# Kernel tuning notes

Hardware: AMD Instinct MI355X
Metric: run time of the kernel (lower is better)

Reference implementation:

```python
import jax, jax.numpy as jnp
import numpy as np

N = 10000       # nodes (atoms)
E = 160000      # edges (avg degree 16)
NE = 10         # num_elements
C = 64          # hidden scalar channels (hidden_irreps 0e multiplicity)
NB = 8          # num_bessel
SH = 9          # spherical-harmonic dim for max_ell=2 (1+3+5)
MLPH = 16       # readout MLP hidden (MLP_irreps)
T = 2           # num_interactions
R_MAX = 5.0
P_CUT = 6       # num_polynomial_cutoff
AVG_NEIGH = 32.0


def _sph(u):
    # real spherical harmonics up to l=2, e3nn 'component' normalization
    x, y, z = u[:, 0], u[:, 1], u[:, 2]
    s3, s5, s15 = 3.0 ** 0.5, 5.0 ** 0.5, 15.0 ** 0.5
    return jnp.stack([
        jnp.ones_like(x),
        s3 * x, s3 * y, s3 * z,
        s15 * x * y, s15 * y * z, (s5 / 2) * (3 * z * z - 1),
        s15 * x * z, (s15 / 2) * (x * x - y * y)], axis=-1)


def _radial(r):
    # Bessel radial basis * smooth polynomial cutoff (RadialEmbeddingBlock)
    n = jnp.arange(1, NB + 1, dtype=r.dtype)
    bessel = (2.0 / R_MAX) ** 0.5 * jnp.sin(n * jnp.pi * r[:, None] / R_MAX) / r[:, None]
    x = jnp.clip(r / R_MAX, 0.0, 1.0)
    p = P_CUT
    fc = (1.0 - 0.5 * (p + 1) * (p + 2) * x ** p
          + p * (p + 2) * x ** (p + 1)
          - 0.5 * p * (p + 1) * x ** (p + 2))
    fc = jnp.where(x < 1.0, fc, 0.0)
    return bessel * fc[:, None]


def setup_inputs():
    key = jax.random.key(0)
    ks = jax.random.split(key, 14)
    positions = jax.random.normal(ks[0], (N, 3), jnp.float32) * 3.0
    node_attrs = jax.nn.one_hot(jax.random.randint(ks[1], (N,), 0, NE), NE, dtype=jnp.float32)
    edge_index = jax.random.randint(ks[2], (2, E), 0, N)
    shifts = jnp.zeros((E, 3), jnp.float32)

    def g(k, shape, fan):
        return jax.random.normal(k, shape, jnp.float32) / np.sqrt(fan)

    params = dict(
        atomic_energies=jax.random.normal(ks[3], (NE,), jnp.float32),
        W_embed=g(ks[4], (NE, C), NE),          # LinearNodeEmbeddingBlock
        W_up=g(ks[5], (T, C, C), C),            # linear_up per interaction
        W_r1=g(ks[6], (T, NB, MLPH), NB),       # radial MLP layer 1
        W_r2=g(ks[7], (T, MLPH, C * SH), MLPH), # radial MLP -> TP weights
        W_mix=g(ks[8], (T, C, SH, C), C * SH),  # post-scatter linear mixing
        W_self=g(ks[9], (T, C, C), C),          # self/skip connection
        w_read=g(ks[10], (C,), C),              # LinearReadoutBlock
        W_mlp1=g(ks[11], (C, MLPH), C),         # NonLinearReadoutBlock
        w_mlp2=g(ks[12], (MLPH,), MLPH),
    )
    return dict(positions=positions, node_attrs=node_attrs, shifts=shifts,
                edge_index=edge_index, **params)


def reference(positions, node_attrs, shifts, atomic_energies, W_embed, W_up,
              W_r1, W_r2, W_mix, W_self, w_read, W_mlp1, w_mlp2, edge_index):
    snd, rcv = edge_index[0], edge_index[1]
    vec = positions[rcv] - positions[snd] + shifts              # [E,3]
    r = jnp.linalg.norm(vec, axis=-1) + 1e-9                    # [E]
    sh = _sph(vec / r[:, None])                                 # [E,SH]
    edge_feats = _radial(r)                                     # [E,NB]

    h = node_attrs @ W_embed                                    # [N,C] node embedding
    reps = [node_attrs @ atomic_energies]                       # node_e0
    for t in range(T):
        h_up = h @ W_up[t]                                      # [N,C]
        # radial-MLP produced tensor-product weights, one per (channel, sh) path
        tp_w = (jax.nn.silu(edge_feats @ W_r1[t]) @ W_r2[t]).reshape(-1, C, SH)
        # gather -> edge-wise tensor product -> scatter-reduce (the hot loop)
        msg = tp_w * h_up[snd][:, :, None] * sh[:, None, :]     # [E,C,SH]
        agg = jax.ops.segment_sum(msg, rcv, num_segments=N) / AVG_NEIGH
        h = jnp.einsum('ncs,cso->no', agg, W_mix[t]) + h @ W_self[t]
        if t < T - 1:
            reps.append(h @ w_read)                             # linear readout
        else:
            reps.append(jax.nn.silu(h @ W_mlp1) @ w_mlp2)       # nonlinear readout
    return jnp.stack(reps, axis=0)  # [T+1, N] per-layer atomic energy contributions
```

## Files before the change

kernel.cpp:

```cpp
#include <hip/hip_runtime.h>
#include <math.h>

#define N_NODES 10000
#define N_EDGES 160000
#define NEL 10
#define C 64
#define NB 8
#define SHD 9
#define MLPH 16
#define CSH 576
#define R_MAX 5.0f
#define INV_AVG 0.03125f
#define SCAN_CH 40
#define ROWP  584
#define NPB   8

typedef _Float16 f16x2 __attribute__((ext_vector_type(2)));
typedef _Float16 f16x8 __attribute__((ext_vector_type(8)));
typedef float    f32x4 __attribute__((ext_vector_type(4)));
typedef _Float16 half_t;

__device__ __forceinline__ float silu_f(float v) {
    return v / (1.0f + __expf(-v));
}

__device__ __forceinline__ float dot2f(f16x2 a, f16x2 b, float c) {
#if __has_builtin(__builtin_amdgcn_fdot2)
    return __builtin_amdgcn_fdot2(a, b, c, false);
#else
    return c + (float)a.x * (float)b.x + (float)a.y * (float)b.y;
#endif
}

__global__ __launch_bounds__(256) void k_zero(
    int* __restrict__ cnt, int* __restrict__ deg)
{
    int i = blockIdx.x * 256 + threadIdx.x;
    if (i == 0) *cnt = 0;
    if (i < N_NODES) deg[i] = 0;
}

__global__ __launch_bounds__(256) void k_edge(
    const float* __restrict__ pos, const float* __restrict__ shifts,
    const int* __restrict__ ei,
    const float* __restrict__ na, const float* __restrict__ We,
    const float* __restrict__ ae,
    const float* __restrict__ Wr2, const float* __restrict__ Wmix,
    const float* __restrict__ Wself, const float* __restrict__ Wup,
    int* __restrict__ cnt, int* __restrict__ deg,
    int* __restrict__ act_snd, int* __restrict__ act_rcv,
    float* __restrict__ act_u, float* __restrict__ act_ef,
    f16x2* __restrict__ wlth, f16x8* __restrict__ wmixf, f16x8* __restrict__ wupf,
    half_t* __restrict__ hh, float* __restrict__ out)
{
    int i = blockIdx.x * 256 + threadIdx.x;
    int lane = threadIdx.x & 63;

    {
        int n = i >> 6;
        float acc = 0.0f, e0 = 0.0f;
        #pragma unroll
        for (int k = 0; k < NEL; k++) {
            float a = na[n * NEL + k];
            acc += a * We[k * C + lane];
            e0 += a * ae[k];
        }
        hh[i] = (half_t)acc;
        if (lane == 0) out[n] = e0;
    }

    if (blockIdx.x >= N_EDGES / 256) {
        int idx = i - N_EDGES;
        if (idx < 2 * 8 * CSH) {
            int t = idx / (8 * CSH);
            int r = idx - t * (8 * CSH);
            int mq = r / CSH, j = r - mq * CSH;
            int c = j & 63, s = j >> 6;
            float lo = Wr2[t * MLPH * CSH + (2 * mq + 0) * CSH + c * SHD + s];
            float hi = Wr2[t * MLPH * CSH + (2 * mq + 1) * CSH + c * SHD + s];
            f16x2 v; v.x = (_Float16)lo; v.y = (_Float16)hi;
            wlth[idx] = v;
        } else if (idx < 2 * 8 * CSH + 10240) {
            int k2 = idx - 2 * 8 * CSH;
            int t = k2 / 5120;
            int r = k2 - t * 5120;
            int ks = r >> 8;
            int rr = r & 255;
            int nt = rr >> 6;
            int ln = rr & 63;
            f16x8 v;
            #pragma unroll
            for (int e = 0; e < 8; e++) {
                int k = ks * 32 + ((ln >> 4) << 3) + e;
                int col = nt * 16 + (ln & 15);
                float x;
                if (k < CSH)
                    x = Wmix[(size_t)t * CSH * C + ((k & 63) * SHD + (k >> 6)) * C + col] * INV_AVG;
                else
                    x = Wself[(size_t)t * C * C + (k - CSH) * C + col];
                v[e] = (_Float16)x;
            }
            wmixf[(size_t)((t * 20 + ks) * 4 + nt) * 64 + ln] = v;
        } else if (idx < 2 * 8 * CSH + 10240 + 1024) {
            int k2 = idx - (2 * 8 * CSH + 10240);
            int t = k2 >> 9;
            int r = k2 & 511;
            int ks = r >> 8;
            int rr = r & 255;
            int nt = rr >> 6;
            int ln = rr & 63;
            f16x8 v;
            #pragma unroll
            for (int e = 0; e < 8; e++) {
                int k = ks * 32 + ((ln >> 4) << 3) + e;
                int col = nt * 16 + (ln & 15);
                v[e] = (_Float16)Wup[(size_t)t * C * C + k * C + col];
            }
            wupf[(size_t)((t * 2 + ks) * 4 + nt) * 64 + ln] = v;
        }
        return;
    }

    int e = i;
    int snd = ei[e];
    int rcv = ei[N_EDGES + e];
    float vx = pos[rcv * 3 + 0] - pos[snd * 3 + 0] + shifts[e * 3 + 0];
    float vy = pos[rcv * 3 + 1] - pos[snd * 3 + 1] + shifts[e * 3 + 1];
    float vz = pos[rcv * 3 + 2] - pos[snd * 3 + 2] + shifts[e * 3 + 2];
    float r = sqrtf(vx * vx + vy * vy + vz * vz) + 1e-9f;
    float x = r / R_MAX;
    bool active = x < 1.0f;

    unsigned long long m = __ballot(active);
    int base = 0;
    if (m) {
        int leader = __ffsll((unsigned long long)m) - 1;
        if (lane == leader) base = atomicAdd(cnt, __popcll(m));
        base = __shfl(base, leader);
    }
    if (!active) return;

    int p = base + __popcll(m & ((1ull << lane) - 1ull));
    act_snd[p] = snd;
    act_rcv[p] = rcv;
    atomicAdd(&deg[rcv], 1);

    float inv_r = 1.0f / r;
    *(float4*)&act_u[p * 4] = make_float4(vx * inv_r, vy * inv_r, vz * inv_r, r);

    float x6 = x * x * x; x6 = x6 * x6;
    float x7 = x6 * x;
    float x8 = x7 * x;
    float fc = 1.0f - 28.0f * x6 + 48.0f * x7 - 21.0f * x8;
    float theta = 3.14159265358979323846f * r / R_MAX;
    float s1 = sinf(theta), c1 = cosf(theta);
    float sn = s1, cn = c1;
    float scale = 0.6324555320336759f * inv_r * fc;
    float ef[NB];
    ef[0] = scale * sn;
    #pragma unroll
    for (int n = 1; n < NB; n++) {
        float sn1 = sn * c1 + cn * s1;
        float cn1 = cn * c1 - sn * s1;
        sn = sn1; cn = cn1;
        ef[n] = scale * sn;
    }
    *(float4*)&act_ef[p * 8 + 0] = make_float4(ef[0], ef[1], ef[2], ef[3]);
    *(float4*)&act_ef[p * 8 + 4] = make_float4(ef[4], ef[5], ef[6], ef[7]);
}

__global__ __launch_bounds__(256) void k_scan(
    const int* __restrict__ deg, int* __restrict__ rowptr, int* __restrict__ cursor)
{
    __shared__ int dl[N_NODES];
    __shared__ int part[256];
    int tid = threadIdx.x;
    for (int i = tid; i < N_NODES; i += 256) dl[i] = deg[i];
    __syncthreads();

    int base = tid * SCAN_CH;
    int s = 0;
    #pragma unroll 8
    for (int i = 0; i < SCAN_CH; i++) {
        int idx = base + i;
        if (idx < N_NODES) s += dl[idx];
    }
    part[tid] = s;
    __syncthreads();
    for (int off = 1; off < 256; off <<= 1) {
        int v = (tid >= off) ? part[tid - off] : 0;
        __syncthreads();
        part[tid] += v;
        __syncthreads();
    }
    int run = part[tid] - s;
    for (int i = 0; i < SCAN_CH; i++) {
        int idx = base + i;
        if (idx < N_NODES) {
            int v = dl[idx];
            dl[idx] = run;
            run += v;
        }
    }
    __syncthreads();
    for (int i = tid; i < N_NODES; i += 256) {
        int r = dl[i];
        rowptr[i] = r;
        cursor[i] = r;
    }
    if (tid == 255) rowptr[N_NODES] = part[255];
}

__global__ __launch_bounds__(256) void k_scatter(
    const int* __restrict__ cnt, const int* __restrict__ act_snd,
    const int* __restrict__ act_rcv, const float* __restrict__ act_u,
    const float* __restrict__ act_ef, const float* __restrict__ Wr1,
    int* __restrict__ cursor,
    int* __restrict__ csnd, int* __restrict__ crcv, float* __restrict__ csh,
    f16x2* __restrict__ chidh0, f16x2* __restrict__ chidh1)
{
    int i = blockIdx.x * 256 + threadIdx.x;
    if (i >= *cnt) return;
    int rcv = act_rcv[i];
    int p = atomicAdd(&cursor[rcv], 1);

    csnd[p] = act_snd[i];
    crcv[p] = rcv;

    float4 u4 = *(const float4*)&act_u[i * 4];
    float ux = u4.x, uy = u4.y, uz = u4.z;
    const float s3 = 1.7320508075688772f;
    const float s5 = 2.23606797749979f;
    const float s15 = 3.872983346207417f;
    *(float4*)&csh[p * 16 + 0] = make_float4(1.0f, s3 * ux, s3 * uy, s3 * uz);
    *(float4*)&csh[p * 16 + 4] = make_float4(s15 * ux * uy, s15 * uy * uz,
                                             0.5f * s5 * (3.0f * uz * uz - 1.0f),
                                             s15 * ux * uz);
    csh[p * 16 + 8] = 0.5f * s15 * (ux * ux - uy * uy);

    float4 e0 = *(const float4*)&act_ef[i * 8 + 0];
    float4 e1 = *(const float4*)&act_ef[i * 8 + 4];
    float ef[NB] = {e0.x, e0.y, e0.z, e0.w, e1.x, e1.y, e1.z, e1.w};

    #pragma unroll
    for (int t = 0; t < 2; t++) {
        f16x2* dst = (t == 0) ? chidh0 : chidh1;
        const float* W = Wr1 + t * NB * MLPH;
        f16x2 hv2[8];
        #pragma unroll
        for (int mp = 0; mp < 8; mp++) {
            float a0 = 0.0f, a1 = 0.0f;
            #pragma unroll
            for (int b = 0; b < NB; b++) {
                float efb = ef[b];
                a0 += efb * W[b * MLPH + 2 * mp + 0];
                a1 += efb * W[b * MLPH + 2 * mp + 1];
            }
            f16x2 v; v.x = (_Float16)silu_f(a0); v.y = (_Float16)silu_f(a1);
            hv2[mp] = v;
        }
        *(float4*)&dst[p * 8 + 0] = *(float4*)&hv2[0];
        *(float4*)&dst[p * 8 + 4] = *(float4*)&hv2[4];
    }
}

__global__ __launch_bounds__(64) void k_upm(
    const half_t* __restrict__ hh, const f16x8* __restrict__ wupf,
    float* __restrict__ hup)
{
    int lane = threadIdx.x & 63;
    int base = blockIdx.x * 16;
    int rowA = base + (lane & 15);
    int kg = (lane >> 4) << 3;

    f32x4 u0 = {0.f,0.f,0.f,0.f}, u1 = {0.f,0.f,0.f,0.f};
    f32x4 u2 = {0.f,0.f,0.f,0.f}, u3 = {0.f,0.f,0.f,0.f};
    const half_t* hrow = hh + (size_t)rowA * C + kg;
    #pragma unroll
    for (int ks = 0; ks < 2; ks++) {
        f16x8 a = *(const f16x8*)(hrow + ks * 32);
        const f16x8* bp = wupf + (size_t)(ks * 4) * 64 + lane;
        u0 = __builtin_amdgcn_mfma_f32_16x16x32_f16(a, bp[0],   u0, 0, 0, 0);
        u1 = __builtin_amdgcn_mfma_f32_16x16x32_f16(a, bp[64],  u1, 0, 0, 0);
        u2 = __builtin_amdgcn_mfma_f32_16x16x32_f16(a, bp[128], u2, 0, 0, 0);
        u3 = __builtin_amdgcn_mfma_f32_16x16x32_f16(a, bp[192], u3, 0, 0, 0);
    }
    int colb = lane & 15;
    int rowb = base + ((lane >> 4) << 2);
    #pragma unroll
    for (int r = 0; r < 4; r++) {
        float* hp = hup + (size_t)(rowb + r) * C + colb;
        hp[0]  = u0[r];
        hp[16] = u1[r];
        hp[32] = u2[r];
        hp[48] = u3[r];
    }
}

template <int RMODE>
__global__ __launch_bounds__(256) void k_fuse(
    const int* __restrict__ rowptr, const int* __restrict__ csnd,
    const int* __restrict__ crcv, const float* __restrict__ csh,
    const f16x2* __restrict__ chh, const f16x2* __restrict__ wlth,
    const float* __restrict__ hup_in, const f16x8* __restrict__ wf,
    const f16x8* __restrict__ wupf1, half_t* __restrict__ hh,
    const float* __restrict__ wread, const float* __restrict__ Wm1,
    const float* __restrict__ wm2,
    float* __restrict__ hup_out, float* __restrict__ rep)
{
    __shared__ half_t Hs[NPB * ROWP];
    __shared__ half_t Hs2[NPB * 72];
    __shared__ float  Hn[NPB * 68];
    __shared__ float  W1l[C * MLPH];

    int lane = threadIdx.x & 63;
    int w = threadIdx.x >> 6;
    int bbase = blockIdx.x * NPB;
    int n0 = bbase + w * 2;
    int beg = rowptr[n0], end = rowptr[n0 + 2];

    f16x2 wreg[8][9];
    #pragma unroll
    for (int mq = 0; mq < 8; mq++)
        #pragma unroll
        for (int jj = 0; jj < 9; jj++)
            wreg[mq][jj] = wlth[mq * CSH + (jj << 6) + lane];

    float acc[9];
    int curRcv = -1;

#define FLUSH() { half_t* ag = &Hs[(curRcv - bbase) * ROWP + lane]; \
    _Pragma("unroll") for (int jj = 0; jj < 9; jj++) ag[jj << 6] = (half_t)acc[jj]; }
#define ZFILL(FROM, TO) for (int zn = (FROM); zn < (TO); zn++) { \
    half_t* ag = &Hs[(zn - bbase) * ROWP + lane]; \
    _Pragma("unroll") for (int jj = 0; jj < 9; jj++) ag[jj << 6] = (half_t)0.0f; }

    for (int k0 = beg; k0 < end; k0 += 4) {
        int nv = end - k0; if (nv > 4) nv = 4;

#define PRE(Q) int kc##Q = (k0 + Q < end) ? k0 + Q : end - 1; \
        int rcvq##Q = crcv[kc##Q]; \
        float hupq##Q = hup_in[csnd[kc##Q] * C + lane];
        PRE(0) PRE(1) PRE(2) PRE(3)
#undef PRE

        float tw0[9], tw1[9], tw2[9], tw3[9];
        #pragma unroll
        for (int jj = 0; jj < 9; jj++) {
            tw0[jj] = 0.f; tw1[jj] = 0.f; tw2[jj] = 0.f; tw3[jj] = 0.f;
        }

        #pragma unroll
        for (int mq = 0; mq < 8; mq++) {
            f16x2 h0 = chh[kc0 * 8 + mq], h1 = chh[kc1 * 8 + mq];
            f16x2 h2 = chh[kc2 * 8 + mq], h3 = chh[kc3 * 8 + mq];
            #pragma unroll
            for (int jj = 0; jj < 9; jj++) {
                f16x2 wv = wreg[mq][jj];
                tw0[jj] = dot2f(h0, wv, tw0[jj]);
                tw1[jj] = dot2f(h1, wv, tw1[jj]);
                tw2[jj] = dot2f(h2, wv, tw2[jj]);
                tw3[jj] = dot2f(h3, wv, tw3[jj]);
            }
        }

#define SCAT(Q) if (Q < nv) { \
        int rcv = rcvq##Q; \
        float hupS = hupq##Q; \
        float4 sA = *(const float4*)&csh[kc##Q * 16]; \
        float4 sB = *(const float4*)&csh[kc##Q * 16 + 4]; \
        float s8v = csh[kc##Q * 16 + 8]; \
        float sh9[9] = {sA.x, sA.y, sA.z, sA.w, sB.x, sB.y, sB.z, sB.w, s8v}; \
        if (rcv != curRcv) { \
            if (curRcv >= 0) { FLUSH(); ZFILL(curRcv + 1, rcv) } else { ZFILL(n0, rcv) } \
            curRcv = rcv; \
            _Pragma("unroll") for (int jj = 0; jj < 9; jj++) acc[jj] = tw##Q[jj] * (hupS * sh9[jj]); \
        } else { \
            _Pragma("unroll") for (int jj = 0; jj < 9; jj++) acc[jj] += tw##Q[jj] * (hupS * sh9[jj]); \
        } }
        SCAT(0) SCAT(1) SCAT(2) SCAT(3)
#undef SCAT
    }

    int zfrom = n0;
    if (curRcv >= 0) { FLUSH(); zfrom = curRcv + 1; }
    ZFILL(zfrom, n0 + 2)
#undef FLUSH
#undef ZFILL

    __syncthreads();

    int rowL = lane & 15;
    int rowS = rowL & 7;
    int kg = (lane >> 4) << 3;
    f32x4 acc4 = {0.f, 0.f, 0.f, 0.f};
    const half_t* hrow = hh + (size_t)(bbase + rowS) * C + kg;
    #pragma unroll
    for (int ks = 0; ks < 20; ks++) {
        f16x8 a = (ks < 18) ? *(const f16x8*)&Hs[rowS * ROWP + ks * 32 + kg]
                            : *(const f16x8*)(hrow + (ks - 18) * 32);
        f16x8 b = wf[(size_t)(ks * 4 + w) * 64 + lane];
        acc4 = __builtin_amdgcn_mfma_f32_16x16x32_f16(a, b, acc4, 0, 0, 0);
    }

    int colb = lane & 15;
    int rq = (lane >> 4) << 2;
    bool storeR = rq < NPB;

    __syncthreads();

    if (RMODE == 0) {
        if (storeR) {
            #pragma unroll
            for (int r = 0; r < 4; r++)
                Hs2[(rq + r) * 72 + w * 16 + colb] = (half_t)acc4[r];
        }
        __syncthreads();

        if (w == 0) {
            int row = lane & 15, seg = lane >> 4;
            float v = 0.0f;
            if (row < NPB) {
                #pragma unroll
                for (int j = 0; j < 16; j++)
                    v += (float)Hs2[row * 72 + seg * 16 + j] * wread[seg * 16 + j];
            }
            v += __shfl_xor(v, 16);
            v += __shfl_xor(v, 32);
            if (seg == 0 && row < NPB) rep[bbase + row] = v;
        }

        {
            int idx = threadIdx.x;
            if (idx < 64) {
                int row = idx >> 3, cq = idx & 7;
                *(float4*)&hh[(size_t)(bbase + row) * C + cq * 8] =
                    *(const float4*)&Hs2[row * 72 + cq * 8];
            }
        }

        f32x4 u = {0.f, 0.f, 0.f, 0.f};
        #pragma unroll
        for (int ks = 0; ks < 2; ks++) {
            f16x8 a = *(const f16x8*)&Hs2[rowS * 72 + ks * 32 + kg];
            f16x8 b = wupf1[(size_t)(ks * 4 + w) * 64 + lane];
            u = __builtin_amdgcn_mfma_f32_16x16x32_f16(a, b, u, 0, 0, 0);
        }
        if (storeR) {
            #pragma unroll
            for (int r = 0; r < 4; r++)
                hup_out[(size_t)(bbase + rq + r) * C + w * 16 + colb] = u[r];
        }
    } else {
        for (int t = threadIdx.x; t < C * MLPH; t += 256) W1l[t] = Wm1[t];
        if (storeR) {
            #pragma unroll
            for (int r = 0; r < 4; r++)
                Hn[(rq + r) * 68 + w * 16 + colb] = acc4[r];
        }
        __syncthreads();

        int n = threadIdx.x >> 4, m = threadIdx.x & 15;
        if (n < NPB) {
            float a2 = 0.0f;
            #pragma unroll 8
            for (int c = 0; c < C; c++) a2 += Hn[n * 68 + c] * W1l[c * MLPH + m];
            float rv = silu_f(a2) * wm2[m];
            rv += __shfl_xor(rv, 1); rv += __shfl_xor(rv, 2);
            rv += __shfl_xor(rv, 4); rv += __shfl_xor(rv, 8);
            if (m == 0) rep[bbase + n] = rv;
        }
    }
}

extern "C" void kernel_launch(void* const* d_in, const int* in_sizes, int n_in,
                              void* d_out, int out_size, void* d_ws, size_t ws_size,
                              hipStream_t stream) {
    const float* pos    = (const float*)d_in[0];
    const float* na     = (const float*)d_in[1];
    const float* shifts = (const float*)d_in[2];
    const int*   ei     = (const int*)d_in[3];
    const float* ae     = (const float*)d_in[4];
    const float* We     = (const float*)d_in[5];
    const float* Wup    = (const float*)d_in[6];
    const float* Wr1    = (const float*)d_in[7];
    const float* Wr2    = (const float*)d_in[8];
    const float* Wmix   = (const float*)d_in[9];
    const float* Wself  = (const float*)d_in[10];
    const float* wread  = (const float*)d_in[11];
    const float* Wm1    = (const float*)d_in[12];
    const float* wm2    = (const float*)d_in[13];
    float* out = (float*)d_out;

    char* ws = (char*)d_ws;
    size_t off = 0;
    auto alloc = [&](size_t bytes) {
        off = (off + 255) & ~(size_t)255;
        void* p = ws + off;
        off += bytes;
        return p;
    };
    int*   cnt     = (int*)alloc(4);
    int*   deg     = (int*)alloc((size_t)N_NODES * 4);
    int*   rowptr  = (int*)alloc((size_t)(N_NODES + 1) * 4);
    int*   cursor  = (int*)alloc((size_t)N_NODES * 4);
    f16x2* wlth    = (f16x2*)alloc((size_t)2 * 8 * CSH * 4);
    f16x8* wmixf   = (f16x8*)alloc((size_t)2 * 5120 * 16);
    f16x8* wupf    = (f16x8*)alloc((size_t)1024 * 16);
    int*   act_snd = (int*)alloc((size_t)N_EDGES * 4);
    int*   act_rcv = (int*)alloc((size_t)N_EDGES * 4);
    float* act_u   = (float*)alloc((size_t)N_EDGES * 4 * 4);
    float* act_ef  = (float*)alloc((size_t)N_EDGES * 8 * 4);
    int*   csnd    = (int*)alloc((size_t)N_EDGES * 4);
    int*   crcv    = (int*)alloc((size_t)N_EDGES * 4);
    float* csh     = (float*)alloc((size_t)N_EDGES * 16 * 4);
    f16x2* chidh0  = (f16x2*)alloc((size_t)N_EDGES * 8 * 4);
    f16x2* chidh1  = (f16x2*)alloc((size_t)N_EDGES * 8 * 4);
    float* hup     = (float*)alloc((size_t)N_NODES * C * 4);
    float* hup2    = (float*)alloc((size_t)N_NODES * C * 4);
    half_t* hh     = (half_t*)alloc((size_t)N_NODES * C * 2);

    k_zero<<<(N_NODES + 255) / 256, 256, 0, stream>>>(cnt, deg);

    k_edge<<<(N_NODES * C) / 256, 256, 0, stream>>>(pos, shifts, ei, na, We, ae,
                                                    Wr2, Wmix, Wself, Wup,
                                                    cnt, deg, act_snd, act_rcv,
                                                    act_u, act_ef,
                                                    wlth, wmixf, wupf, hh, out);
    k_upm<<<N_NODES / 16, 64, 0, stream>>>(hh, wupf, hup);
    k_scan<<<1, 256, 0, stream>>>(deg, rowptr, cursor);
    k_scatter<<<N_EDGES / 256, 256, 0, stream>>>(cnt, act_snd, act_rcv,
                                                 act_u, act_ef, Wr1, cursor,
                                                 csnd, crcv, csh, chidh0, chidh1);

    k_fuse<0><<<N_NODES / NPB, 256, 0, stream>>>(rowptr, csnd, crcv, csh,
                                                 chidh0, wlth, hup,
                                                 wmixf, wupf + 512, hh,
                                                 wread, Wm1, wm2,
                                                 hup2, out + N_NODES);

    k_fuse<1><<<N_NODES / NPB, 256, 0, stream>>>(rowptr, csnd, crcv, csh,
                                                 chidh1, wlth + 8 * CSH, hup2,
                                                 wmixf + 5120, wupf + 512, hh,
                                                 wread, Wm1, wm2,
                                                 hup, out + 2 * N_NODES);
}
```

Before: 124.6 us.

## Build degree histogram in scan LDS, fold up-projection into scatter, widen fuse tiles

The per-receiver degree count is no longer done with global atomics in the edge kernel. The single-block scan kernel now builds it with shared-memory atomics over the compacted receiver list, so the deg buffer and its zeroing go away. The standalone up-projection MFMA kernel is merged into the scatter kernel as extra trailing waves, saving a launch. The fused interaction kernel now handles 16 nodes per block instead of 8, which fills all 16 MFMA rows and removes the row masking, but it halves the block count and gives each wave twice as many edges to walk. The trade-off is that histogram work now runs serially inside one block.

```diff
diff --git a/kernel.cpp b/kernel.cpp
--- a/kernel.cpp
+++ b/kernel.cpp
@@ -13,7 +13,6 @@
 #define INV_AVG 0.03125f
 #define SCAN_CH 40
 #define ROWP  584
-#define NPB   8
 
 typedef _Float16 f16x2 __attribute__((ext_vector_type(2)));
 typedef _Float16 f16x8 __attribute__((ext_vector_type(8)));
@@ -32,12 +31,9 @@
 #endif
 }
 
-__global__ __launch_bounds__(256) void k_zero(
-    int* __restrict__ cnt, int* __restrict__ deg)
+__global__ __launch_bounds__(64) void k_zero(int* __restrict__ cnt)
 {
-    int i = blockIdx.x * 256 + threadIdx.x;
-    if (i == 0) *cnt = 0;
-    if (i < N_NODES) deg[i] = 0;
+    if (threadIdx.x == 0) *cnt = 0;
 }
 
 __global__ __launch_bounds__(256) void k_edge(
@@ -47,7 +43,7 @@
     const float* __restrict__ ae,
     const float* __restrict__ Wr2, const float* __restrict__ Wmix,
     const float* __restrict__ Wself, const float* __restrict__ Wup,
-    int* __restrict__ cnt, int* __restrict__ deg,
+    int* __restrict__ cnt,
     int* __restrict__ act_snd, int* __restrict__ act_rcv,
     float* __restrict__ act_u, float* __restrict__ act_ef,
     f16x2* __restrict__ wlth, f16x8* __restrict__ wmixf, f16x8* __restrict__ wupf,
@@ -143,7 +139,6 @@
     int p = base + __popcll(m & ((1ull << lane) - 1ull));
     act_snd[p] = snd;
     act_rcv[p] = rcv;
-    atomicAdd(&deg[rcv], 1);
 
     float inv_r = 1.0f / r;
     *(float4*)&act_u[p * 4] = make_float4(vx * inv_r, vy * inv_r, vz * inv_r, r);
@@ -170,12 +165,17 @@
 }
 
 __global__ __launch_bounds__(256) void k_scan(
-    const int* __restrict__ deg, int* __restrict__ rowptr, int* __restrict__ cursor)
+    const int* __restrict__ cnt, const int* __restrict__ act_rcv,
+    int* __restrict__ rowptr, int* __restrict__ cursor)
 {
     __shared__ int dl[N_NODES];
     __shared__ int part[256];
     int tid = threadIdx.x;
-    for (int i = tid; i < N_NODES; i += 256) dl[i] = deg[i];
+    for (int i = tid; i < N_NODES; i += 256) dl[i] = 0;
+    __syncthreads();
+
+    int nAct = *cnt;
+    for (int i = tid; i < nAct; i += 256) atomicAdd(&dl[act_rcv[i]], 1);
     __syncthreads();
 
     int base = tid * SCAN_CH;
@@ -215,12 +215,51 @@
     const int* __restrict__ cnt, const int* __restrict__ act_snd,
     const int* __restrict__ act_rcv, const float* __restrict__ act_u,
     const float* __restrict__ act_ef, const float* __restrict__ Wr1,
+    const half_t* __restrict__ hh, const f16x8* __restrict__ wupf,
     int* __restrict__ cursor,
     int* __restrict__ csnd, int* __restrict__ crcv, float* __restrict__ csh,
-    f16x2* __restrict__ chidh0, f16x2* __restrict__ chidh1)
+    f16x2* __restrict__ chidh0, f16x2* __restrict__ chidh1,
+    float* __restrict__ hup)
 {
     int i = blockIdx.x * 256 + threadIdx.x;
-    if (i >= *cnt) return;
+    int nAct = *cnt;
+    int wGlobal = i >> 6;
+    int nActW = (nAct + 63) >> 6;
+
+    if (wGlobal >= nActW) {
+        int F = wGlobal - nActW;
+        if (F >= N_NODES / 16) return;
+        int lane = threadIdx.x & 63;
+        int base = F * 16;
+        int rowA = base + (lane & 15);
+        int kg = (lane >> 4) << 3;
+
+        f32x4 u0 = {0.f,0.f,0.f,0.f}, u1 = {0.f,0.f,0.f,0.f};
+        f32x4 u2 = {0.f,0.f,0.f,0.f}, u3 = {0.f,0.f,0.f,0.f};
+        const half_t* hrow = hh + (size_t)rowA * C + kg;
+        #pragma unroll
+        for (int ks = 0; ks < 2; ks++) {
+            f16x8 a = *(const f16x8*)(hrow + ks * 32);
+            const f16x8* bp = wupf + (size_t)(ks * 4) * 64 + lane;
+            u0 = __builtin_amdgcn_mfma_f32_16x16x32_f16(a, bp[0],   u0, 0, 0, 0);
+            u1 = __builtin_amdgcn_mfma_f32_16x16x32_f16(a, bp[64],  u1, 0, 0, 0);
+            u2 = __builtin_amdgcn_mfma_f32_16x16x32_f16(a, bp[128], u2, 0, 0, 0);
+            u3 = __builtin_amdgcn_mfma_f32_16x16x32_f16(a, bp[192], u3, 0, 0, 0);
+        }
+        int colb = lane & 15;
+        int rowb = base + ((lane >> 4) << 2);
+        #pragma unroll
+        for (int r = 0; r < 4; r++) {
+            float* hp = hup + (size_t)(rowb + r) * C + colb;
+            hp[0]  = u0[r];
+            hp[16] = u1[r];
+            hp[32] = u2[r];
+            hp[48] = u3[r];
+        }
+        return;
+    }
+
+    if (i >= nAct) return;
     int rcv = act_rcv[i];
     int p = atomicAdd(&cursor[rcv], 1);
 
@@ -261,39 +300,6 @@
         }
         *(float4*)&dst[p * 8 + 0] = *(float4*)&hv2[0];
         *(float4*)&dst[p * 8 + 4] = *(float4*)&hv2[4];
-    }
-}
-
-__global__ __launch_bounds__(64) void k_upm(
-    const half_t* __restrict__ hh, const f16x8* __restrict__ wupf,
-    float* __restrict__ hup)
-{
-    int lane = threadIdx.x & 63;
-    int base = blockIdx.x * 16;
-    int rowA = base + (lane & 15);
-    int kg = (lane >> 4) << 3;
-
-    f32x4 u0 = {0.f,0.f,0.f,0.f}, u1 = {0.f,0.f,0.f,0.f};
-    f32x4 u2 = {0.f,0.f,0.f,0.f}, u3 = {0.f,0.f,0.f,0.f};
-    const half_t* hrow = hh + (size_t)rowA * C + kg;
-    #pragma unroll
-    for (int ks = 0; ks < 2; ks++) {
-        f16x8 a = *(const f16x8*)(hrow + ks * 32);
-        const f16x8* bp = wupf + (size_t)(ks * 4) * 64 + lane;
-        u0 = __builtin_amdgcn_mfma_f32_16x16x32_f16(a, bp[0],   u0, 0, 0, 0);
-        u1 = __builtin_amdgcn_mfma_f32_16x16x32_f16(a, bp[64],  u1, 0, 0, 0);
-        u2 = __builtin_amdgcn_mfma_f32_16x16x32_f16(a, bp[128], u2, 0, 0, 0);
-        u3 = __builtin_amdgcn_mfma_f32_16x16x32_f16(a, bp[192], u3, 0, 0, 0);
-    }
-    int colb = lane & 15;
-    int rowb = base + ((lane >> 4) << 2);
-    #pragma unroll
-    for (int r = 0; r < 4; r++) {
-        float* hp = hup + (size_t)(rowb + r) * C + colb;
-        hp[0]  = u0[r];
-        hp[16] = u1[r];
-        hp[32] = u2[r];
-        hp[48] = u3[r];
     }
 }
 
@@ -308,16 +314,14 @@
     const float* __restrict__ wm2,
     float* __restrict__ hup_out, float* __restrict__ rep)
 {
-    __shared__ half_t Hs[NPB * ROWP];
-    __shared__ half_t Hs2[NPB * 72];
-    __shared__ float  Hn[NPB * 68];
-    __shared__ float  W1l[C * MLPH];
+    __shared__ half_t Hs[16 * ROWP];
+    __shared__ half_t Hs2[16 * 72];
 
     int lane = threadIdx.x & 63;
     int w = threadIdx.x >> 6;
-    int bbase = blockIdx.x * NPB;
-    int n0 = bbase + w * 2;
-    int beg = rowptr[n0], end = rowptr[n0 + 2];
+    int bbase = blockIdx.x * 16;
+    int n0 = bbase + w * 4;
+    int beg = rowptr[n0], end = rowptr[n0 + 4];
 
     f16x2 wreg[8][9];
     #pragma unroll
@@ -384,20 +388,19 @@
 
     int zfrom = n0;
     if (curRcv >= 0) { FLUSH(); zfrom = curRcv + 1; }
-    ZFILL(zfrom, n0 + 2)
+    ZFILL(zfrom, n0 + 4)
 #undef FLUSH
 #undef ZFILL
 
     __syncthreads();
 
     int rowL = lane & 15;
-    int rowS = rowL & 7;
     int kg = (lane >> 4) << 3;
     f32x4 acc4 = {0.f, 0.f, 0.f, 0.f};
-    const half_t* hrow = hh + (size_t)(bbase + rowS) * C + kg;
+    const half_t* hrow = hh + (size_t)(bbase + rowL) * C + kg;
     #pragma unroll
     for (int ks = 0; ks < 20; ks++) {
-        f16x8 a = (ks < 18) ? *(const f16x8*)&Hs[rowS * ROWP + ks * 32 + kg]
+        f16x8 a = (ks < 18) ? *(const f16x8*)&Hs[rowL * ROWP + ks * 32 + kg]
                             : *(const f16x8*)(hrow + (ks - 18) * 32);
         f16x8 b = wf[(size_t)(ks * 4 + w) * 64 + lane];
         acc4 = __builtin_amdgcn_mfma_f32_16x16x32_f16(a, b, acc4, 0, 0, 0);
@@ -405,34 +408,29 @@
 
     int colb = lane & 15;
     int rq = (lane >> 4) << 2;
-    bool storeR = rq < NPB;
 
     __syncthreads();
 
     if (RMODE == 0) {
-        if (storeR) {
-            #pragma unroll
-            for (int r = 0; r < 4; r++)
-                Hs2[(rq + r) * 72 + w * 16 + colb] = (half_t)acc4[r];
-        }
+        #pragma unroll
+        for (int r = 0; r < 4; r++)
+            Hs2[(rq + r) * 72 + w * 16 + colb] = (half_t)acc4[r];
         __syncthreads();
 
         if (w == 0) {
             int row = lane & 15, seg = lane >> 4;
             float v = 0.0f;
-            if (row < NPB) {
-                #pragma unroll
-                for (int j = 0; j < 16; j++)
-                    v += (float)Hs2[row * 72 + seg * 16 + j] * wread[seg * 16 + j];
-            }
+            #pragma unroll
+            for (int j = 0; j < 16; j++)
+                v += (float)Hs2[row * 72 + seg * 16 + j] * wread[seg * 16 + j];
             v += __shfl_xor(v, 16);
             v += __shfl_xor(v, 32);
-            if (seg == 0 && row < NPB) rep[bbase + row] = v;
+            if (seg == 0) rep[bbase + row] = v;
         }
 
         {
             int idx = threadIdx.x;
-            if (idx < 64) {
+            if (idx < 128) {
                 int row = idx >> 3, cq = idx & 7;
                 *(float4*)&hh[(size_t)(bbase + row) * C + cq * 8] =
                     *(const float4*)&Hs2[row * 72 + cq * 8];
@@ -442,34 +440,30 @@
         f32x4 u = {0.f, 0.f, 0.f, 0.f};
         #pragma unroll
         for (int ks = 0; ks < 2; ks++) {
-            f16x8 a = *(const f16x8*)&Hs2[rowS * 72 + ks * 32 + kg];
+            f16x8 a = *(const f16x8*)&Hs2[rowL * 72 + ks * 32 + kg];
             f16x8 b = wupf1[(size_t)(ks * 4 + w) * 64 + lane];
             u = __builtin_amdgcn_mfma_f32_16x16x32_f16(a, b, u, 0, 0, 0);
         }
-        if (storeR) {
-            #pragma unroll
-            for (int r = 0; r < 4; r++)
-                hup_out[(size_t)(bbase + rq + r) * C + w * 16 + colb] = u[r];
-        }
+        #pragma unroll
+        for (int r = 0; r < 4; r++)
+            hup_out[(size_t)(bbase + rq + r) * C + w * 16 + colb] = u[r];
     } else {
+        float* Hn = (float*)Hs;
+        float* W1l = (float*)Hs + 16 * 68;
         for (int t = threadIdx.x; t < C * MLPH; t += 256) W1l[t] = Wm1[t];
-        if (storeR) {
-            #pragma unroll
-            for (int r = 0; r < 4; r++)
-                Hn[(rq + r) * 68 + w * 16 + colb] = acc4[r];
-        }
+        #pragma unroll
+        for (int r = 0; r < 4; r++)
+            Hn[(rq + r) * 68 + w * 16 + colb] = acc4[r];
         __syncthreads();
 
         int n = threadIdx.x >> 4, m = threadIdx.x & 15;
-        if (n < NPB) {
-            float a2 = 0.0f;
-            #pragma unroll 8
-            for (int c = 0; c < C; c++) a2 += Hn[n * 68 + c] * W1l[c * MLPH + m];
-            float rv = silu_f(a2) * wm2[m];
-            rv += __shfl_xor(rv, 1); rv += __shfl_xor(rv, 2);
-            rv += __shfl_xor(rv, 4); rv += __shfl_xor(rv, 8);
-            if (m == 0) rep[bbase + n] = rv;
-        }
+        float a2 = 0.0f;
+        #pragma unroll 8
+        for (int c = 0; c < C; c++) a2 += Hn[n * 68 + c] * W1l[c * MLPH + m];
+        float rv = silu_f(a2) * wm2[m];
+        rv += __shfl_xor(rv, 1); rv += __shfl_xor(rv, 2);
+        rv += __shfl_xor(rv, 4); rv += __shfl_xor(rv, 8);
+        if (m == 0) rep[bbase + n] = rv;
     }
 }
 
@@ -501,7 +495,6 @@
         return p;
     };
     int*   cnt     = (int*)alloc(4);
-    int*   deg     = (int*)alloc((size_t)N_NODES * 4);
     int*   rowptr  = (int*)alloc((size_t)(N_NODES + 1) * 4);
     int*   cursor  = (int*)alloc((size_t)N_NODES * 4);
     f16x2* wlth    = (f16x2*)alloc((size_t)2 * 8 * CSH * 4);
@@ -520,28 +513,28 @@
     float* hup2    = (float*)alloc((size_t)N_NODES * C * 4);
     half_t* hh     = (half_t*)alloc((size_t)N_NODES * C * 2);
 
-    k_zero<<<(N_NODES + 255) / 256, 256, 0, stream>>>(cnt, deg);
+    k_zero<<<1, 64, 0, stream>>>(cnt);
 
     k_edge<<<(N_NODES * C) / 256, 256, 0, stream>>>(pos, shifts, ei, na, We, ae,
                                                     Wr2, Wmix, Wself, Wup,
-                                                    cnt, deg, act_snd, act_rcv,
+                                                    cnt, act_snd, act_rcv,
                                                     act_u, act_ef,
                                                     wlth, wmixf, wupf, hh, out);
-    k_upm<<<N_NODES / 16, 64, 0, stream>>>(hh, wupf, hup);
-    k_scan<<<1, 256, 0, stream>>>(deg, rowptr, cursor);
+    k_scan<<<1, 256, 0, stream>>>(cnt, act_rcv, rowptr, cursor);
     k_scatter<<<N_EDGES / 256, 256, 0, stream>>>(cnt, act_snd, act_rcv,
-                                                 act_u, act_ef, Wr1, cursor,
-                                                 csnd, crcv, csh, chidh0, chidh1);
-
-    k_fuse<0><<<N_NODES / NPB, 256, 0, stream>>>(rowptr, csnd, crcv, csh,
-                                                 chidh0, wlth, hup,
-                                                 wmixf, wupf + 512, hh,
-                                                 wread, Wm1, wm2,
-                                                 hup2, out + N_NODES);
-
-    k_fuse<1><<<N_NODES / NPB, 256, 0, stream>>>(rowptr, csnd, crcv, csh,
-                                                 chidh1, wlth + 8 * CSH, hup2,
-                                                 wmixf + 5120, wupf + 512, hh,
-                                                 wread, Wm1, wm2,
-                                                 hup, out + 2 * N_NODES);
-}
+                                                 act_u, act_ef, Wr1, hh, wupf,
+                                                 cursor, csnd, crcv, csh,
+                                                 chidh0, chidh1, hup);
+
+    k_fuse<0><<<N_NODES / 16, 256, 0, stream>>>(rowptr, csnd, crcv, csh,
+                                                chidh0, wlth, hup,
+                                                wmixf, wupf + 512, hh,
+                                                wread, Wm1, wm2,
+                                                hup2, out + N_NODES);
+
+    k_fuse<1><<<N_NODES / 16, 256, 0, stream>>>(rowptr, csnd, crcv, csh,
+                                                chidh1, wlth + 8 * CSH, hup2,
+                                                wmixf + 5120, wupf + 512, hh,
+                                                wread, Wm1, wm2,
+                                                hup, out + 2 * N_NODES);
+}
```

Result: slower. 156.2 us (+25.4%).
